# Kernel tuning notes

Hardware: AMD Instinct MI355X
Metric: run time of the kernel (lower is better)

The kernel has to match this reference:

```python
import jax, jax.numpy as jnp
import numpy as np

B, L, D_IN, D_MODEL, N_STATE, DT_RANK, K = 2, 2048, 512, 1024, 16, 64, 4


def setup_inputs() -> dict:
    key = jax.random.key(0)
    ks = jax.random.split(key, 12)
    s = 0.02
    inp = {
        "x_in": jax.random.normal(ks[0], (B, L, D_IN), dtype=jnp.float32),
        "W_in": jax.random.normal(ks[1], (D_MODEL, D_IN), dtype=jnp.float32) * s,
        "W_res": jax.random.normal(ks[2], (D_MODEL, D_IN), dtype=jnp.float32) * s,
        "W_out": jax.random.normal(ks[3], (D_IN, D_MODEL), dtype=jnp.float32) * s,
        "conv_w": jax.random.normal(ks[4], (D_MODEL, 1, K), dtype=jnp.float32) * 0.2,
        "conv_b": jax.random.normal(ks[5], (D_MODEL,), dtype=jnp.float32) * 0.02,
        "A_log": jnp.broadcast_to(jnp.log(jnp.arange(1, N_STATE + 1, dtype=jnp.float32)), (D_MODEL, N_STATE)).copy(),
        "D_param": jnp.ones((D_MODEL,), dtype=jnp.float32),
        "W_B": jax.random.normal(ks[6], (N_STATE, D_MODEL), dtype=jnp.float32) * s,
        "W_C": jax.random.normal(ks[7], (N_STATE, D_MODEL), dtype=jnp.float32) * s,
        "W_dt": jax.random.normal(ks[8], (DT_RANK, D_MODEL), dtype=jnp.float32) * s,
        "W_dtproj": jax.random.normal(ks[9], (D_MODEL, DT_RANK), dtype=jnp.float32) * s,
        "b_dtproj": jax.random.normal(ks[10], (D_MODEL,), dtype=jnp.float32) * 0.05,
    }
    return inp


def _mamba(x_in, W_in, W_res, W_out, conv_w, conv_b, A_log, D_param, W_B, W_C, W_dt, W_dtproj, b_dtproj):
    d_model = conv_w.shape[0]
    k = conv_w.shape[-1]
    x = jnp.einsum('bld,md->blm', x_in, W_in)           # (B,L,D)
    res = jnp.einsum('bld,md->blm', x_in, W_res)        # (B,L,D)
    # causal depthwise conv1d (pad k-1 left, truncate to L == torch pad+slice)
    xc = jnp.transpose(x, (0, 2, 1))                     # (B,D,L)
    xc = jax.lax.conv_general_dilated(xc, conv_w, window_strides=(1,), padding=[(k - 1, 0)],
                                      feature_group_count=d_model,
                                      dimension_numbers=('NCH', 'OIH', 'NCH'))
    xc = xc + conv_b[None, :, None]
    x = jax.nn.silu(jnp.transpose(xc, (0, 2, 1)))        # (B,L,D)
    # selective SSM
    A = -jnp.exp(A_log)                                  # (D,N)
    Bp = jnp.einsum('bld,nd->bln', x, W_B)               # (B,L,N)
    Cp = jnp.einsum('bld,nd->bln', x, W_C)               # (B,L,N)
    delta = jax.nn.softplus(jnp.einsum('bld,rd->blr', x, W_dt) @ W_dtproj.T + b_dtproj)  # (B,L,D)
    dA = jnp.exp(delta[..., None] * A)                   # (B,L,D,N)
    dBu = (delta * x)[..., None] * Bp[:, :, None, :]     # (B,L,D,N)

    def step(h, inp):
        dA_t, dBu_t, C_t = inp
        h = dA_t * h + dBu_t                             # (B,D,N)
        y_t = jnp.einsum('bdn,bn->bd', h, C_t)
        return h, y_t

    h0 = jnp.zeros((x.shape[0], d_model, A.shape[1]), dtype=x.dtype)
    _, ys = jax.lax.scan(step, h0, (jnp.swapaxes(dA, 0, 1), jnp.swapaxes(dBu, 0, 1), jnp.swapaxes(Cp, 0, 1)))
    y = jnp.swapaxes(ys, 0, 1) + x * D_param             # (B,L,D)
    y = y * jax.nn.silu(res)
    return jnp.einsum('bld,od->blo', y, W_out)


def reference(x_in, W_in, W_res, W_out, conv_w, conv_b, A_log, D_param, W_B, W_C, W_dt, W_dtproj, b_dtproj):
    return _mamba(x_in, W_in, W_res, W_out, conv_w, conv_b, A_log, D_param, W_B, W_C, W_dt, W_dtproj, b_dtproj)
```

## Files before the change

kernel.cpp:

```cpp
#include <hip/hip_runtime.h>
#include <stdint.h>
#include <stddef.h>

#define DEVFN __device__ __forceinline__

typedef short bf16x8 __attribute__((ext_vector_type(8)));
typedef short s16x4 __attribute__((ext_vector_type(4)));
typedef float f32x4 __attribute__((ext_vector_type(4)));

namespace {
constexpr int kB   = 2;
constexpr int kL   = 2048;
constexpr int kDin = 512;
constexpr int kDm  = 1024;
constexpr int kNs  = 16;
constexpr int kDtr = 64;
constexpr int kR   = kB * kL;
constexpr int kCH  = 128;
constexpr int kLC  = kL / kCH;
}

DEVFN unsigned short f2bf(float f) {
  union { float f; unsigned u; } v; v.f = f;
  unsigned u = v.u + 0x7fffu + ((v.u >> 16) & 1u);
  return (unsigned short)(u >> 16);
}

DEVFN float bf2f(unsigned short s) {
  union { unsigned u; float f; } v; v.u = ((unsigned)s) << 16;
  return v.f;
}

DEVFN void async16(const void* g, void* l) {
  __builtin_amdgcn_global_load_lds(
      (const __attribute__((address_space(1))) void*)g,
      (__attribute__((address_space(3))) void*)l, 16, 0, 0);
}

DEVFN float sigm(float x) { return 1.0f / (1.0f + __expf(-x)); }

__global__ void prep_kernel(const float* __restrict__ x_in, const float* __restrict__ W_in,
                            const float* __restrict__ W_res, const float* __restrict__ W_out,
                            const float* __restrict__ W_dtp, const float* __restrict__ W_B,
                            const float* __restrict__ W_C, const float* __restrict__ W_dt,
                            const float* __restrict__ A_log,
                            unsigned short* __restrict__ Xb, unsigned short* __restrict__ Wirb,
                            unsigned short* __restrict__ Woutb,
                            unsigned short* __restrict__ Wdtpb, unsigned short* __restrict__ BCdtb,
                            float* __restrict__ Aneg) {
  int i = blockIdx.x * 256 + threadIdx.x;
  if (i < kR * kDin) { Xb[i] = f2bf(x_in[i]); return; }
  i -= kR * kDin;
  if (i < 2 * kDm * kDin) {
    Wirb[i] = f2bf(i < kDm * kDin ? W_in[i] : W_res[i - kDm * kDin]);
    return;
  }
  i -= 2 * kDm * kDin;
  if (i < kDin * kDm) { Woutb[i] = f2bf(W_out[i]); return; }
  i -= kDin * kDm;
  if (i < kDm * kDtr) { Wdtpb[i] = f2bf(W_dtp[i]); return; }
  i -= kDm * kDtr;
  if (i < 128 * kDm) {
    int rr = i >> 10, kk = i & 1023;
    float v = 0.f;
    if (rr < 16)      v = W_B[rr * kDm + kk];
    else if (rr < 32) v = W_C[(rr - 16) * kDm + kk];
    else if (rr < 96) v = W_dt[(rr - 32) * kDm + kk];
    BCdtb[i] = f2bf(v);
    return;
  }
  i -= 128 * kDm;
  if (i < kDm * kNs) { Aneg[i] = -__expf(A_log[i]); }
}

template <int EPI>
__global__ __launch_bounds__(256) void gemm_nt(const unsigned short* __restrict__ A,
                                               const unsigned short* __restrict__ Bw,
                                               float* __restrict__ C,
                                               const float* __restrict__ bias,
                                               unsigned short* __restrict__ Z,
                                               int M, int N, int K) {
  __shared__ __align__(16) unsigned short As[2][128 * 32];
  __shared__ __align__(16) unsigned short Bs[2][128 * 32];
  const int tid = threadIdx.x;
  const int w = tid >> 6, lane = tid & 63;
  const int ntiles = N >> 7;
  const int mt = blockIdx.x / ntiles, nt = blockIdx.x - mt * ntiles;
  const int row0 = mt << 7, col0 = nt << 7;
  const int wr = w >> 1, wc = w & 1;
  const int lr = lane & 15, hi = lane >> 4;

  const int s0 = w * 128 + lane;
  const int s1 = s0 + 64;
  const int c0s = s0 >> 7, r0s = s0 & 127;
  const int c1s = s1 >> 7, r1s = s1 & 127;

  f32x4 acc[4][4] = {};

  auto stage = [&](int buf, int kt) {
    const int kb = kt * 32;
    async16(A  + (size_t)(row0 + r0s) * K + kb + c0s * 8, (void*)&As[buf][(w * 128) * 8]);
    async16(A  + (size_t)(row0 + r1s) * K + kb + c1s * 8, (void*)&As[buf][(w * 128 + 64) * 8]);
    async16(Bw + (size_t)(col0 + r0s) * K + kb + c0s * 8, (void*)&Bs[buf][(w * 128) * 8]);
    async16(Bw + (size_t)(col0 + r1s) * K + kb + c1s * 8, (void*)&Bs[buf][(w * 128 + 64) * 8]);
  };

  const int KT = K >> 5;
  stage(0, 0);
  __syncthreads();
  int buf = 0;
  for (int kt = 0; kt < KT; ++kt) {
    if (kt + 1 < KT) stage(buf ^ 1, kt + 1);
    bf16x8 af[4], bfr[4];
#pragma unroll
    for (int i = 0; i < 4; ++i) {
      af[i]  = *(const bf16x8*)&As[buf][(hi * 128 + wr * 64 + i * 16 + lr) * 8];
      bfr[i] = *(const bf16x8*)&Bs[buf][(hi * 128 + wc * 64 + i * 16 + lr) * 8];
    }
#pragma unroll
    for (int i = 0; i < 4; ++i)
#pragma unroll
      for (int j = 0; j < 4; ++j)
        acc[i][j] = __builtin_amdgcn_mfma_f32_16x16x32_bf16(af[i], bfr[j], acc[i][j], 0, 0, 0);
    __syncthreads();
    buf ^= 1;
  }

#pragma unroll
  for (int i = 0; i < 4; ++i) {
#pragma unroll
    for (int j = 0; j < 4; ++j) {
#pragma unroll
      for (int q = 0; q < 4; ++q) {
        const int r  = row0 + wr * 64 + i * 16 + hi * 4 + q;
        const int cc = col0 + wc * 64 + j * 16 + lr;
        float v = acc[i][j][q];
        if (EPI == 1) {
          v += bias[cc];
          v = fmaxf(v, 0.f) + log1pf(__expf(-fabsf(v)));
          Z[(size_t)r * kDm + cc] = f2bf(v);
        } else if (EPI == 4) {
          if (cc < kDm) C[(size_t)r * kDm + cc] = v;
          else          Z[(size_t)r * kDm + (cc - kDm)] = f2bf(v * sigm(v));
        } else {
          C[(size_t)r * N + cc] = v;
        }
      }
    }
  }
}

__global__ __launch_bounds__(256) void gemm_bcz(const unsigned short* __restrict__ A,
                                                const unsigned short* __restrict__ Bw,
                                                float* __restrict__ P) {
  __shared__ __align__(16) unsigned short As[2][128 * 32];
  __shared__ __align__(16) unsigned short Bs[2][128 * 32];
  const int tid = threadIdx.x;
  const int w = tid >> 6, lane = tid & 63;
  const int mtiles = kR >> 7;
  const int ks = blockIdx.x / mtiles;
  const int mt = blockIdx.x - ks * mtiles;
  const int row0 = mt << 7;
  const int kbase = ks * (kDm / 4);
  const int wr = w >> 1, wc = w & 1;
  const int lr = lane & 15, hi = lane >> 4;

  const int s0 = w * 128 + lane;
  const int s1 = s0 + 64;
  const int c0s = s0 >> 7, r0s = s0 & 127;
  const int c1s = s1 >> 7, r1s = s1 & 127;

  f32x4 acc[4][4] = {};

  auto stage = [&](int buf, int kt) {
    const int kb = kbase + kt * 32;
    async16(A  + (size_t)(row0 + r0s) * kDm + kb + c0s * 8, (void*)&As[buf][(w * 128) * 8]);
    async16(A  + (size_t)(row0 + r1s) * kDm + kb + c1s * 8, (void*)&As[buf][(w * 128 + 64) * 8]);
    async16(Bw + (size_t)r0s * kDm + kb + c0s * 8, (void*)&Bs[buf][(w * 128) * 8]);
    async16(Bw + (size_t)r1s * kDm + kb + c1s * 8, (void*)&Bs[buf][(w * 128 + 64) * 8]);
  };

  const int KT = (kDm / 4) >> 5;
  stage(0, 0);
  __syncthreads();
  int buf = 0;
  for (int kt = 0; kt < KT; ++kt) {
    if (kt + 1 < KT) stage(buf ^ 1, kt + 1);
    bf16x8 af[4], bfr[4];
#pragma unroll
    for (int i = 0; i < 4; ++i) {
      af[i]  = *(const bf16x8*)&As[buf][(hi * 128 + wr * 64 + i * 16 + lr) * 8];
      bfr[i] = *(const bf16x8*)&Bs[buf][(hi * 128 + wc * 64 + i * 16 + lr) * 8];
    }
#pragma unroll
    for (int i = 0; i < 4; ++i)
#pragma unroll
      for (int j = 0; j < 4; ++j)
        acc[i][j] = __builtin_amdgcn_mfma_f32_16x16x32_bf16(af[i], bfr[j], acc[i][j], 0, 0, 0);
    __syncthreads();
    buf ^= 1;
  }

  float* Pk = P + (size_t)ks * kR * 128;
#pragma unroll
  for (int i = 0; i < 4; ++i)
#pragma unroll
    for (int j = 0; j < 4; ++j)
#pragma unroll
      for (int q = 0; q < 4; ++q) {
        const int r  = row0 + wr * 64 + i * 16 + hi * 4 + q;
        const int cc = wc * 64 + j * 16 + lr;
        Pk[(size_t)r * 128 + cc] = acc[i][j][q];
      }
}

__global__ __launch_bounds__(256) void bcz_reduce(const float* __restrict__ P,
                                                  float* __restrict__ BCz,
                                                  unsigned short* __restrict__ z1b) {
  const int i4 = blockIdx.x * 256 + threadIdx.x;
  const size_t base = (size_t)i4 * 4;
  const size_t stride = (size_t)kR * 128;
  f32x4 s = *(const f32x4*)(P + base);
  s += *(const f32x4*)(P + base + stride);
  s += *(const f32x4*)(P + base + 2 * stride);
  s += *(const f32x4*)(P + base + 3 * stride);
  *(f32x4*)(BCz + base) = s;
  const int cc = (int)(base & 127);
  if (cc >= 32 && cc < 96) {
    const int r = (int)(base >> 7);
    s16x4 z = { (short)f2bf(s.x), (short)f2bf(s.y), (short)f2bf(s.z), (short)f2bf(s.w) };
    *(s16x4*)(z1b + (size_t)r * kDtr + (cc - 32)) = z;
  }
}

__global__ __launch_bounds__(256) void conv_silu_kernel(const float* __restrict__ xf,
                                                        const float* __restrict__ conv_w,
                                                        const float* __restrict__ conv_b,
                                                        unsigned short* __restrict__ xcb) {
  const int i = blockIdx.x * 256 + threadIdx.x;
  const int d = i & (kDm - 1);
  const int r = i >> 10;
  const int l = r & (kL - 1);
  float s = conv_b[d];
#pragma unroll
  for (int j = 0; j < 4; ++j) {
    const int ls = l - 3 + j;
    if (ls >= 0) s += xf[(size_t)i + (j - 3) * kDm] * conv_w[d * 4 + j];
  }
  const float v = s * sigm(s);
  xcb[i] = f2bf(v);
}

__global__ __launch_bounds__(256) void scan_phase1(const unsigned short* __restrict__ deltab,
                                                   const unsigned short* __restrict__ xcb,
                                                   const float* __restrict__ BCz,
                                                   float* __restrict__ hend,
                                                   float* __restrict__ dtsum) {
  __shared__ float Bsh[kLC][kNs];
  const int tid = threadIdx.x;
  const int dblk = blockIdx.x & 15;
  const int bc = blockIdx.x >> 4;
  const int c = bc & (kCH - 1);
  const int b = bc >> 7;
  const int rbase = b * kL + c * kLC;
  Bsh[tid >> 4][tid & 15] = BCz[(size_t)(rbase + (tid >> 4)) * 128 + (tid & 15)];
  __syncthreads();

  const int s = tid & 3, dl = tid >> 2;
  const int d = (dblk << 6) + dl;
  const size_t colbase = (size_t)rbase * kDm + d;
  float h0 = 0.f, h1 = 0.f, h2 = 0.f, h3 = 0.f, S = 0.f;
  float dtn = bf2f(deltab[colbase]);
  float xvn = bf2f(xcb[colbase]);
  for (int t = 0; t < kLC; ++t) {
    const float dt = dtn, xv = xvn;
    if (t + 1 < kLC) {
      dtn = bf2f(deltab[colbase + (size_t)(t + 1) * kDm]);
      xvn = bf2f(xcb[colbase + (size_t)(t + 1) * kDm]);
    }
    S += dt;
    const float e1 = __expf(-dt);
    const float e2 = e1 * e1, e4 = e2 * e2, e8 = e4 * e4;
    float pb = e1;
    if (s & 1) pb *= e4;
    if (s & 2) pb *= e8;
    const float f1 = pb * e1, f2 = f1 * e1, f3 = f2 * e1;
    const float du = dt * xv;
    const f32x4 Bv = *(const f32x4*)&Bsh[t][s << 2];
    h0 = fmaf(pb, h0, du * Bv.x);
    h1 = fmaf(f1, h1, du * Bv.y);
    h2 = fmaf(f2, h2, du * Bv.z);
    h3 = fmaf(f3, h3, du * Bv.w);
  }
  const size_t o = ((size_t)bc << 14) + ((size_t)d << 4) + (s << 2);
  *(f32x4*)(hend + o) = f32x4{h0, h1, h2, h3};
  if (s == 0) dtsum[(size_t)bc * kDm + d] = S;
}

__global__ __launch_bounds__(256) void scan_phase2(const float* __restrict__ hend,
                                                   const float* __restrict__ dtsum,
                                                   const float* __restrict__ Aneg,
                                                   float* __restrict__ hin) {
  const int flat = blockIdx.x * 256 + threadIdx.x;
  const int dn = flat & (kDm * kNs - 1);
  const int b = flat >> 14;
  const int d = dn >> 4;
  const float Ar = Aneg[dn];
  size_t o = (size_t)b * kCH * (kDm * kNs) + dn;
  size_t sb = (size_t)b * kCH * kDm + d;
  float h = 0.f;
  float he = hend[o];
  float pp = __expf(Ar * dtsum[sb]);
  for (int c = 0; c < kCH; ++c) {
    const float heC = he, pC = pp;
    if (c + 1 < kCH) {
      he = hend[o + kDm * kNs];
      pp = __expf(Ar * dtsum[sb + kDm]);
    }
    hin[o] = h;
    h = fmaf(pC, h, heC);
    o += kDm * kNs;
    sb += kDm;
  }
}

__global__ __launch_bounds__(256) void scan_phase3(const unsigned short* __restrict__ deltab,
                                                   const unsigned short* __restrict__ xcb,
                                                   const unsigned short* __restrict__ resb,
                                                   const float* __restrict__ BCz,
                                                   const float* __restrict__ hin,
                                                   const float* __restrict__ D_param,
                                                   unsigned short* __restrict__ yb) {
  __shared__ float BCs[kLC][32];
  __shared__ unsigned short ysh[kLC][64];
  const int tid = threadIdx.x;
  const int dblk = blockIdx.x & 15;
  const int bc = blockIdx.x >> 4;
  const int c = bc & (kCH - 1);
  const int b = bc >> 7;
  const int rbase = b * kL + c * kLC;
#pragma unroll
  for (int k2 = 0; k2 < 2; ++k2) {
    const int idx = tid + k2 * 256;
    BCs[idx >> 5][idx & 31] = BCz[(size_t)(rbase + (idx >> 5)) * 128 + (idx & 31)];
  }
  __syncthreads();

  const int s = tid & 3, dl = tid >> 2;
  const int d = (dblk << 6) + dl;
  const size_t colbase = (size_t)rbase * kDm + d;
  const size_t o = ((size_t)bc << 14) + ((size_t)d << 4) + (s << 2);
  const f32x4 hv = *(const f32x4*)(hin + o);
  float h0 = hv.x, h1 = hv.y, h2 = hv.z, h3 = hv.w;
  const float Dp = D_param[d];
  float dtn = bf2f(deltab[colbase]);
  float xvn = bf2f(xcb[colbase]);
  float rsn = bf2f(resb[colbase]);
  for (int t = 0; t < kLC; ++t) {
    const float dt = dtn, xv = xvn, sres = rsn;
    if (t + 1 < kLC) {
      dtn = bf2f(deltab[colbase + (size_t)(t + 1) * kDm]);
      xvn = bf2f(xcb[colbase + (size_t)(t + 1) * kDm]);
      rsn = bf2f(resb[colbase + (size_t)(t + 1) * kDm]);
    }
    const float e1 = __expf(-dt);
    const float e2 = e1 * e1, e4 = e2 * e2, e8 = e4 * e4;
    float pb = e1;
    if (s & 1) pb *= e4;
    if (s & 2) pb *= e8;
    const float f1 = pb * e1, f2 = f1 * e1, f3 = f2 * e1;
    const float du = dt * xv;
    const f32x4 Bv = *(const f32x4*)&BCs[t][s << 2];
    const f32x4 Cv = *(const f32x4*)&BCs[t][16 + (s << 2)];
    h0 = fmaf(pb, h0, du * Bv.x);
    h1 = fmaf(f1, h1, du * Bv.y);
    h2 = fmaf(f2, h2, du * Bv.z);
    h3 = fmaf(f3, h3, du * Bv.w);
    float y = h0 * Cv.x + h1 * Cv.y + h2 * Cv.z + h3 * Cv.w;
    y += __shfl_xor(y, 1);
    y += __shfl_xor(y, 2);
    if (s == 0) ysh[t][dl] = f2bf((y + xv * Dp) * sres);
  }
  __syncthreads();
#pragma unroll
  for (int k2 = 0; k2 < 4; ++k2) {
    const int idx = tid + k2 * 256;
    const int tt = idx >> 6, dd = idx & 63;
    yb[(size_t)(rbase + tt) * kDm + (dblk << 6) + dd] = ysh[tt][dd];
  }
}

extern "C" void kernel_launch(void* const* d_in, const int* in_sizes, int n_in,
                              void* d_out, int out_size, void* d_ws, size_t ws_size,
                              hipStream_t stream) {
  const float* x_in   = (const float*)d_in[0];
  const float* W_in   = (const float*)d_in[1];
  const float* W_res  = (const float*)d_in[2];
  const float* W_out  = (const float*)d_in[3];
  const float* conv_w = (const float*)d_in[4];
  const float* conv_b = (const float*)d_in[5];
  const float* A_log  = (const float*)d_in[6];
  const float* D_par  = (const float*)d_in[7];
  const float* W_B    = (const float*)d_in[8];
  const float* W_C    = (const float*)d_in[9];
  const float* W_dt   = (const float*)d_in[10];
  const float* W_dtp  = (const float*)d_in[11];
  const float* b_dtp  = (const float*)d_in[12];
  float* out = (float*)d_out;

  char* p = (char*)d_ws;
  auto alloc = [&](size_t bytes) { void* q = (void*)p; p += (bytes + 255) & ~(size_t)255; return q; };

  float* xf    = (float*)alloc(sizeof(float) * (size_t)kR * kDm);
  float* BCz   = (float*)alloc(sizeof(float) * (size_t)kR * 128);
  float* Ppart = (float*)alloc(sizeof(float) * 4ull * kR * 128);
  float* hend  = (float*)alloc(sizeof(float) * (size_t)kB * kCH * kDm * kNs);
  float* hin   = (float*)alloc(sizeof(float) * (size_t)kB * kCH * kDm * kNs);
  float* dtsum = (float*)alloc(sizeof(float) * (size_t)kB * kCH * kDm);
  float* Aneg  = (float*)alloc(sizeof(float) * (size_t)kDm * kNs);
  unsigned short* Xb     = (unsigned short*)alloc(2ull * kR * kDin);
  unsigned short* xcb    = (unsigned short*)alloc(2ull * kR * kDm);
  unsigned short* yb     = (unsigned short*)alloc(2ull * kR * kDm);
  unsigned short* resb   = (unsigned short*)alloc(2ull * kR * kDm);
  unsigned short* deltab = (unsigned short*)alloc(2ull * kR * kDm);
  unsigned short* z1b    = (unsigned short*)alloc(2ull * kR * kDtr);
  unsigned short* Wirb   = (unsigned short*)alloc(2ull * 2 * kDm * kDin);
  unsigned short* Woutb  = (unsigned short*)alloc(2ull * kDin * kDm);
  unsigned short* Wdtpb  = (unsigned short*)alloc(2ull * kDm * kDtr);
  unsigned short* BCdtb  = (unsigned short*)alloc(2ull * 128 * kDm);

  if ((size_t)(p - (char*)d_ws) > ws_size) return;

  {
    const int total = kR * kDin + 2 * kDm * kDin + kDin * kDm + kDm * kDtr + 128 * kDm + kDm * kNs;
    prep_kernel<<<(total + 255) / 256, 256, 0, stream>>>(
        x_in, W_in, W_res, W_out, W_dtp, W_B, W_C, W_dt, A_log,
        Xb, Wirb, Woutb, Wdtpb, BCdtb, Aneg);
  }
  gemm_nt<4><<<(kR / 128) * (2 * kDm / 128), 256, 0, stream>>>(Xb, Wirb, xf, nullptr, resb, kR, 2 * kDm, kDin);
  conv_silu_kernel<<<(kR * kDm) / 256, 256, 0, stream>>>(xf, conv_w, conv_b, xcb);
  gemm_bcz<<<4 * (kR / 128), 256, 0, stream>>>(xcb, BCdtb, Ppart);
  bcz_reduce<<<(kR * 128 / 4) / 256, 256, 0, stream>>>(Ppart, BCz, z1b);
  gemm_nt<1><<<(kR / 128) * (kDm / 128), 256, 0, stream>>>(z1b, Wdtpb, nullptr, b_dtp, deltab, kR, kDm, kDtr);
  scan_phase1<<<kB * kCH * (kDm / 64), 256, 0, stream>>>(deltab, xcb, BCz, hend, dtsum);
  scan_phase2<<<(kB * kDm * kNs) / 256, 256, 0, stream>>>(hend, dtsum, Aneg, hin);
  scan_phase3<<<kB * kCH * (kDm / 64), 256, 0, stream>>>(deltab, xcb, resb, BCz, hin, D_par, yb);
  gemm_nt<0><<<(kR / 128) * (kDin / 128), 256, 0, stream>>>(yb, Woutb, out, nullptr, nullptr, kR, kDin, kDm);
}
```

Measured before the change: 174.7 us.

## Fold dt low-rank into packed weight, bf16 intermediates, vectorized conv, smaller out tiles

Precomputes W_dtproj·W_dt as a 1024x1024 bf16 matrix and packs it with W_B/W_C into one 1152-wide weight. A single GEMM then yields delta (with softplus) and B/C, replacing the split-K BC GEMM, its reduce kernel and the rank-64 dt GEMM. The x projection is stored as bf16 and the conv runs 8 channels per thread with vector loads. Scan chunk states (hend/hin) are kept in bf16, phase2 uses 128-thread blocks, and the output GEMM uses 64-row tiles for more blocks. These changes add FLOPs in the dt path and lose precision in the chunk states and the fused dt weight.

```diff
diff --git a/kernel.cpp b/kernel.cpp
--- a/kernel.cpp
+++ b/kernel.cpp
@@ -18,6 +18,7 @@
 constexpr int kR   = kB * kL;
 constexpr int kCH  = 128;
 constexpr int kLC  = kL / kCH;
+constexpr int kNp  = 1152;
 }
 
 DEVFN unsigned short f2bf(float f) {
@@ -46,7 +47,8 @@
                             const float* __restrict__ A_log,
                             unsigned short* __restrict__ Xb, unsigned short* __restrict__ Wirb,
                             unsigned short* __restrict__ Woutb,
-                            unsigned short* __restrict__ Wdtpb, unsigned short* __restrict__ BCdtb,
+                            unsigned short* __restrict__ Wdtpb, unsigned short* __restrict__ WdtT,
+                            unsigned short* __restrict__ Wpack,
                             float* __restrict__ Aneg) {
   int i = blockIdx.x * 256 + threadIdx.x;
   if (i < kR * kDin) { Xb[i] = f2bf(x_in[i]); return; }
@@ -60,13 +62,18 @@
   i -= kDin * kDm;
   if (i < kDm * kDtr) { Wdtpb[i] = f2bf(W_dtp[i]); return; }
   i -= kDm * kDtr;
+  if (i < kDm * kDtr) {
+    const int d = i >> 6, t = i & 63;
+    WdtT[i] = f2bf(W_dt[t * kDm + d]);
+    return;
+  }
+  i -= kDm * kDtr;
   if (i < 128 * kDm) {
-    int rr = i >> 10, kk = i & 1023;
+    const int rr = i >> 10, kk = i & 1023;
     float v = 0.f;
     if (rr < 16)      v = W_B[rr * kDm + kk];
     else if (rr < 32) v = W_C[(rr - 16) * kDm + kk];
-    else if (rr < 96) v = W_dt[(rr - 32) * kDm + kk];
-    BCdtb[i] = f2bf(v);
+    Wpack[(size_t)(1024 + rr) * kDm + kk] = f2bf(v);
     return;
   }
   i -= 128 * kDm;
@@ -79,6 +86,7 @@
                                                float* __restrict__ C,
                                                const float* __restrict__ bias,
                                                unsigned short* __restrict__ Z,
+                                               unsigned short* __restrict__ Z2,
                                                int M, int N, int K) {
   __shared__ __align__(16) unsigned short As[2][128 * 32];
   __shared__ __align__(16) unsigned short Bs[2][128 * 32];
@@ -135,65 +143,66 @@
         const int r  = row0 + wr * 64 + i * 16 + hi * 4 + q;
         const int cc = col0 + wc * 64 + j * 16 + lr;
         float v = acc[i][j][q];
-        if (EPI == 1) {
-          v += bias[cc];
-          v = fmaxf(v, 0.f) + log1pf(__expf(-fabsf(v)));
-          Z[(size_t)r * kDm + cc] = f2bf(v);
-        } else if (EPI == 4) {
-          if (cc < kDm) C[(size_t)r * kDm + cc] = v;
-          else          Z[(size_t)r * kDm + (cc - kDm)] = f2bf(v * sigm(v));
-        } else {
-          C[(size_t)r * N + cc] = v;
+        if (EPI == 4) {
+          if (cc < kDm) Z[(size_t)r * kDm + cc] = f2bf(v);
+          else          Z2[(size_t)r * kDm + (cc - kDm)] = f2bf(v * sigm(v));
+        } else if (EPI == 5) {
+          Z[(size_t)r * N + cc] = f2bf(v);
+        } else if (EPI == 6) {
+          if (cc < 1024) {
+            v += bias[cc];
+            v = fmaxf(v, 0.f) + log1pf(__expf(-fabsf(v)));
+            Z[(size_t)r * kDm + cc] = f2bf(v);
+          } else if (cc < 1056) {
+            C[(size_t)r * 32 + (cc - 1024)] = v;
+          }
         }
       }
     }
   }
 }
 
-__global__ __launch_bounds__(256) void gemm_bcz(const unsigned short* __restrict__ A,
-                                                const unsigned short* __restrict__ Bw,
-                                                float* __restrict__ P) {
-  __shared__ __align__(16) unsigned short As[2][128 * 32];
+__global__ __launch_bounds__(256) void gemm_out64(const unsigned short* __restrict__ A,
+                                                  const unsigned short* __restrict__ Bw,
+                                                  float* __restrict__ C) {
+  __shared__ __align__(16) unsigned short As[2][64 * 32];
   __shared__ __align__(16) unsigned short Bs[2][128 * 32];
   const int tid = threadIdx.x;
   const int w = tid >> 6, lane = tid & 63;
-  const int mtiles = kR >> 7;
-  const int ks = blockIdx.x / mtiles;
-  const int mt = blockIdx.x - ks * mtiles;
-  const int row0 = mt << 7;
-  const int kbase = ks * (kDm / 4);
+  const int mt = blockIdx.x >> 2, nt = blockIdx.x & 3;
+  const int row0 = mt << 6, col0 = nt << 7;
   const int wr = w >> 1, wc = w & 1;
   const int lr = lane & 15, hi = lane >> 4;
 
-  const int s0 = w * 128 + lane;
-  const int s1 = s0 + 64;
+  const int cA = tid >> 6, rA = tid & 63;
+  const int s0 = w * 128 + lane, s1 = s0 + 64;
   const int c0s = s0 >> 7, r0s = s0 & 127;
   const int c1s = s1 >> 7, r1s = s1 & 127;
 
-  f32x4 acc[4][4] = {};
+  f32x4 acc[2][4] = {};
 
   auto stage = [&](int buf, int kt) {
-    const int kb = kbase + kt * 32;
-    async16(A  + (size_t)(row0 + r0s) * kDm + kb + c0s * 8, (void*)&As[buf][(w * 128) * 8]);
-    async16(A  + (size_t)(row0 + r1s) * kDm + kb + c1s * 8, (void*)&As[buf][(w * 128 + 64) * 8]);
-    async16(Bw + (size_t)r0s * kDm + kb + c0s * 8, (void*)&Bs[buf][(w * 128) * 8]);
-    async16(Bw + (size_t)r1s * kDm + kb + c1s * 8, (void*)&Bs[buf][(w * 128 + 64) * 8]);
+    const int kb = kt * 32;
+    async16(A  + (size_t)(row0 + rA) * kDm + kb + cA * 8, (void*)&As[buf][tid * 8]);
+    async16(Bw + (size_t)(col0 + r0s) * kDm + kb + c0s * 8, (void*)&Bs[buf][(w * 128) * 8]);
+    async16(Bw + (size_t)(col0 + r1s) * kDm + kb + c1s * 8, (void*)&Bs[buf][(w * 128 + 64) * 8]);
   };
 
-  const int KT = (kDm / 4) >> 5;
+  const int KT = kDm >> 5;
   stage(0, 0);
   __syncthreads();
   int buf = 0;
   for (int kt = 0; kt < KT; ++kt) {
     if (kt + 1 < KT) stage(buf ^ 1, kt + 1);
-    bf16x8 af[4], bfr[4];
-#pragma unroll
-    for (int i = 0; i < 4; ++i) {
-      af[i]  = *(const bf16x8*)&As[buf][(hi * 128 + wr * 64 + i * 16 + lr) * 8];
-      bfr[i] = *(const bf16x8*)&Bs[buf][(hi * 128 + wc * 64 + i * 16 + lr) * 8];
-    }
-#pragma unroll
-    for (int i = 0; i < 4; ++i)
+    bf16x8 af[2], bfr[4];
+#pragma unroll
+    for (int i = 0; i < 2; ++i)
+      af[i] = *(const bf16x8*)&As[buf][(hi * 64 + wr * 32 + i * 16 + lr) * 8];
+#pragma unroll
+    for (int j = 0; j < 4; ++j)
+      bfr[j] = *(const bf16x8*)&Bs[buf][(hi * 128 + wc * 64 + j * 16 + lr) * 8];
+#pragma unroll
+    for (int i = 0; i < 2; ++i)
 #pragma unroll
       for (int j = 0; j < 4; ++j)
         acc[i][j] = __builtin_amdgcn_mfma_f32_16x16x32_bf16(af[i], bfr[j], acc[i][j], 0, 0, 0);
@@ -201,60 +210,51 @@
     buf ^= 1;
   }
 
-  float* Pk = P + (size_t)ks * kR * 128;
-#pragma unroll
-  for (int i = 0; i < 4; ++i)
+#pragma unroll
+  for (int i = 0; i < 2; ++i)
 #pragma unroll
     for (int j = 0; j < 4; ++j)
 #pragma unroll
       for (int q = 0; q < 4; ++q) {
-        const int r  = row0 + wr * 64 + i * 16 + hi * 4 + q;
-        const int cc = wc * 64 + j * 16 + lr;
-        Pk[(size_t)r * 128 + cc] = acc[i][j][q];
+        const int r  = row0 + wr * 32 + i * 16 + hi * 4 + q;
+        const int cc = col0 + wc * 64 + j * 16 + lr;
+        C[(size_t)r * kDin + cc] = acc[i][j][q];
       }
 }
 
-__global__ __launch_bounds__(256) void bcz_reduce(const float* __restrict__ P,
-                                                  float* __restrict__ BCz,
-                                                  unsigned short* __restrict__ z1b) {
-  const int i4 = blockIdx.x * 256 + threadIdx.x;
-  const size_t base = (size_t)i4 * 4;
-  const size_t stride = (size_t)kR * 128;
-  f32x4 s = *(const f32x4*)(P + base);
-  s += *(const f32x4*)(P + base + stride);
-  s += *(const f32x4*)(P + base + 2 * stride);
-  s += *(const f32x4*)(P + base + 3 * stride);
-  *(f32x4*)(BCz + base) = s;
-  const int cc = (int)(base & 127);
-  if (cc >= 32 && cc < 96) {
-    const int r = (int)(base >> 7);
-    s16x4 z = { (short)f2bf(s.x), (short)f2bf(s.y), (short)f2bf(s.z), (short)f2bf(s.w) };
-    *(s16x4*)(z1b + (size_t)r * kDtr + (cc - 32)) = z;
-  }
-}
-
-__global__ __launch_bounds__(256) void conv_silu_kernel(const float* __restrict__ xf,
-                                                        const float* __restrict__ conv_w,
-                                                        const float* __restrict__ conv_b,
-                                                        unsigned short* __restrict__ xcb) {
-  const int i = blockIdx.x * 256 + threadIdx.x;
-  const int d = i & (kDm - 1);
-  const int r = i >> 10;
+__global__ __launch_bounds__(256) void conv8_kernel(const unsigned short* __restrict__ xfb,
+                                                    const float* __restrict__ conv_w,
+                                                    const float* __restrict__ conv_b,
+                                                    unsigned short* __restrict__ xcb) {
+  const int i8 = blockIdx.x * 256 + threadIdx.x;
+  const int r = i8 >> 7;
+  const int d0 = (i8 & 127) << 3;
   const int l = r & (kL - 1);
-  float s = conv_b[d];
+  bf16x8 xr[4];
 #pragma unroll
   for (int j = 0; j < 4; ++j) {
     const int ls = l - 3 + j;
-    if (ls >= 0) s += xf[(size_t)i + (j - 3) * kDm] * conv_w[d * 4 + j];
-  }
-  const float v = s * sigm(s);
-  xcb[i] = f2bf(v);
+    if (ls >= 0) xr[j] = *(const bf16x8*)(xfb + (size_t)(r - 3 + j) * kDm + d0);
+    else         xr[j] = bf16x8{};
+  }
+  bf16x8 outv;
+#pragma unroll
+  for (int e = 0; e < 8; ++e) {
+    const f32x4 wv = *(const f32x4*)(conv_w + (d0 + e) * 4);
+    float s = conv_b[d0 + e];
+    s = fmaf(bf2f((unsigned short)xr[0][e]), wv.x, s);
+    s = fmaf(bf2f((unsigned short)xr[1][e]), wv.y, s);
+    s = fmaf(bf2f((unsigned short)xr[2][e]), wv.z, s);
+    s = fmaf(bf2f((unsigned short)xr[3][e]), wv.w, s);
+    outv[e] = (short)f2bf(s * sigm(s));
+  }
+  *(bf16x8*)(xcb + (size_t)r * kDm + d0) = outv;
 }
 
 __global__ __launch_bounds__(256) void scan_phase1(const unsigned short* __restrict__ deltab,
                                                    const unsigned short* __restrict__ xcb,
-                                                   const float* __restrict__ BCz,
-                                                   float* __restrict__ hend,
+                                                   const float* __restrict__ BC,
+                                                   unsigned short* __restrict__ hendb,
                                                    float* __restrict__ dtsum) {
   __shared__ float Bsh[kLC][kNs];
   const int tid = threadIdx.x;
@@ -263,7 +263,7 @@
   const int c = bc & (kCH - 1);
   const int b = bc >> 7;
   const int rbase = b * kL + c * kLC;
-  Bsh[tid >> 4][tid & 15] = BCz[(size_t)(rbase + (tid >> 4)) * 128 + (tid & 15)];
+  Bsh[tid >> 4][tid & 15] = BC[(size_t)(rbase + (tid >> 4)) * 32 + (tid & 15)];
   __syncthreads();
 
   const int s = tid & 3, dl = tid >> 2;
@@ -293,15 +293,15 @@
     h3 = fmaf(f3, h3, du * Bv.w);
   }
   const size_t o = ((size_t)bc << 14) + ((size_t)d << 4) + (s << 2);
-  *(f32x4*)(hend + o) = f32x4{h0, h1, h2, h3};
+  *(s16x4*)(hendb + o) = s16x4{(short)f2bf(h0), (short)f2bf(h1), (short)f2bf(h2), (short)f2bf(h3)};
   if (s == 0) dtsum[(size_t)bc * kDm + d] = S;
 }
 
-__global__ __launch_bounds__(256) void scan_phase2(const float* __restrict__ hend,
+__global__ __launch_bounds__(128) void scan_phase2(const unsigned short* __restrict__ hendb,
                                                    const float* __restrict__ dtsum,
                                                    const float* __restrict__ Aneg,
-                                                   float* __restrict__ hin) {
-  const int flat = blockIdx.x * 256 + threadIdx.x;
+                                                   unsigned short* __restrict__ hinb) {
+  const int flat = blockIdx.x * 128 + threadIdx.x;
   const int dn = flat & (kDm * kNs - 1);
   const int b = flat >> 14;
   const int d = dn >> 4;
@@ -309,15 +309,15 @@
   size_t o = (size_t)b * kCH * (kDm * kNs) + dn;
   size_t sb = (size_t)b * kCH * kDm + d;
   float h = 0.f;
-  float he = hend[o];
+  float he = bf2f(hendb[o]);
   float pp = __expf(Ar * dtsum[sb]);
   for (int c = 0; c < kCH; ++c) {
     const float heC = he, pC = pp;
     if (c + 1 < kCH) {
-      he = hend[o + kDm * kNs];
+      he = bf2f(hendb[o + kDm * kNs]);
       pp = __expf(Ar * dtsum[sb + kDm]);
     }
-    hin[o] = h;
+    hinb[o] = f2bf(h);
     h = fmaf(pC, h, heC);
     o += kDm * kNs;
     sb += kDm;
@@ -327,8 +327,8 @@
 __global__ __launch_bounds__(256) void scan_phase3(const unsigned short* __restrict__ deltab,
                                                    const unsigned short* __restrict__ xcb,
                                                    const unsigned short* __restrict__ resb,
-                                                   const float* __restrict__ BCz,
-                                                   const float* __restrict__ hin,
+                                                   const float* __restrict__ BC,
+                                                   const unsigned short* __restrict__ hinb,
                                                    const float* __restrict__ D_param,
                                                    unsigned short* __restrict__ yb) {
   __shared__ float BCs[kLC][32];
@@ -342,7 +342,7 @@
 #pragma unroll
   for (int k2 = 0; k2 < 2; ++k2) {
     const int idx = tid + k2 * 256;
-    BCs[idx >> 5][idx & 31] = BCz[(size_t)(rbase + (idx >> 5)) * 128 + (idx & 31)];
+    BCs[idx >> 5][idx & 31] = BC[(size_t)(rbase + (idx >> 5)) * 32 + (idx & 31)];
   }
   __syncthreads();
 
@@ -350,8 +350,9 @@
   const int d = (dblk << 6) + dl;
   const size_t colbase = (size_t)rbase * kDm + d;
   const size_t o = ((size_t)bc << 14) + ((size_t)d << 4) + (s << 2);
-  const f32x4 hv = *(const f32x4*)(hin + o);
-  float h0 = hv.x, h1 = hv.y, h2 = hv.z, h3 = hv.w;
+  const s16x4 hv = *(const s16x4*)(hinb + o);
+  float h0 = bf2f((unsigned short)hv[0]), h1 = bf2f((unsigned short)hv[1]);
+  float h2 = bf2f((unsigned short)hv[2]), h3 = bf2f((unsigned short)hv[3]);
   const float Dp = D_param[d];
   float dtn = bf2f(deltab[colbase]);
   float xvn = bf2f(xcb[colbase]);
@@ -411,39 +412,37 @@
   char* p = (char*)d_ws;
   auto alloc = [&](size_t bytes) { void* q = (void*)p; p += (bytes + 255) & ~(size_t)255; return q; };
 
-  float* xf    = (float*)alloc(sizeof(float) * (size_t)kR * kDm);
-  float* BCz   = (float*)alloc(sizeof(float) * (size_t)kR * 128);
-  float* Ppart = (float*)alloc(sizeof(float) * 4ull * kR * 128);
-  float* hend  = (float*)alloc(sizeof(float) * (size_t)kB * kCH * kDm * kNs);
-  float* hin   = (float*)alloc(sizeof(float) * (size_t)kB * kCH * kDm * kNs);
+  float* BC    = (float*)alloc(sizeof(float) * (size_t)kR * 32);
   float* dtsum = (float*)alloc(sizeof(float) * (size_t)kB * kCH * kDm);
   float* Aneg  = (float*)alloc(sizeof(float) * (size_t)kDm * kNs);
+  unsigned short* hendb  = (unsigned short*)alloc(2ull * kB * kCH * kDm * kNs);
+  unsigned short* hinb   = (unsigned short*)alloc(2ull * kB * kCH * kDm * kNs);
   unsigned short* Xb     = (unsigned short*)alloc(2ull * kR * kDin);
+  unsigned short* xfb    = (unsigned short*)alloc(2ull * kR * kDm);
   unsigned short* xcb    = (unsigned short*)alloc(2ull * kR * kDm);
   unsigned short* yb     = (unsigned short*)alloc(2ull * kR * kDm);
   unsigned short* resb   = (unsigned short*)alloc(2ull * kR * kDm);
   unsigned short* deltab = (unsigned short*)alloc(2ull * kR * kDm);
-  unsigned short* z1b    = (unsigned short*)alloc(2ull * kR * kDtr);
   unsigned short* Wirb   = (unsigned short*)alloc(2ull * 2 * kDm * kDin);
   unsigned short* Woutb  = (unsigned short*)alloc(2ull * kDin * kDm);
   unsigned short* Wdtpb  = (unsigned short*)alloc(2ull * kDm * kDtr);
-  unsigned short* BCdtb  = (unsigned short*)alloc(2ull * 128 * kDm);
+  unsigned short* WdtT   = (unsigned short*)alloc(2ull * kDm * kDtr);
+  unsigned short* Wpack  = (unsigned short*)alloc(2ull * kNp * kDm);
 
   if ((size_t)(p - (char*)d_ws) > ws_size) return;
 
   {
-    const int total = kR * kDin + 2 * kDm * kDin + kDin * kDm + kDm * kDtr + 128 * kDm + kDm * kNs;
+    const int total = kR * kDin + 2 * kDm * kDin + kDin * kDm + 2 * kDm * kDtr + 128 * kDm + kDm * kNs;
     prep_kernel<<<(total + 255) / 256, 256, 0, stream>>>(
         x_in, W_in, W_res, W_out, W_dtp, W_B, W_C, W_dt, A_log,
-        Xb, Wirb, Woutb, Wdtpb, BCdtb, Aneg);
-  }
-  gemm_nt<4><<<(kR / 128) * (2 * kDm / 128), 256, 0, stream>>>(Xb, Wirb, xf, nullptr, resb, kR, 2 * kDm, kDin);
-  conv_silu_kernel<<<(kR * kDm) / 256, 256, 0, stream>>>(xf, conv_w, conv_b, xcb);
-  gemm_bcz<<<4 * (kR / 128), 256, 0, stream>>>(xcb, BCdtb, Ppart);
-  bcz_reduce<<<(kR * 128 / 4) / 256, 256, 0, stream>>>(Ppart, BCz, z1b);
-  gemm_nt<1><<<(kR / 128) * (kDm / 128), 256, 0, stream>>>(z1b, Wdtpb, nullptr, b_dtp, deltab, kR, kDm, kDtr);
-  scan_phase1<<<kB * kCH * (kDm / 64), 256, 0, stream>>>(deltab, xcb, BCz, hend, dtsum);
-  scan_phase2<<<(kB * kDm * kNs) / 256, 256, 0, stream>>>(hend, dtsum, Aneg, hin);
-  scan_phase3<<<kB * kCH * (kDm / 64), 256, 0, stream>>>(deltab, xcb, resb, BCz, hin, D_par, yb);
-  gemm_nt<0><<<(kR / 128) * (kDin / 128), 256, 0, stream>>>(yb, Woutb, out, nullptr, nullptr, kR, kDin, kDm);
-}
+        Xb, Wirb, Woutb, Wdtpb, WdtT, Wpack, Aneg);
+  }
+  gemm_nt<5><<<(kDm / 128) * (kDm / 128), 256, 0, stream>>>(Wdtpb, WdtT, nullptr, nullptr, Wpack, nullptr, kDm, kDm, kDtr);
+  gemm_nt<4><<<(kR / 128) * (2 * kDm / 128), 256, 0, stream>>>(Xb, Wirb, nullptr, nullptr, xfb, resb, kR, 2 * kDm, kDin);
+  conv8_kernel<<<(kR * kDm / 8) / 256, 256, 0, stream>>>(xfb, conv_w, conv_b, xcb);
+  gemm_nt<6><<<(kR / 128) * (kNp / 128), 256, 0, stream>>>(xcb, Wpack, BC, b_dtp, deltab, nullptr, kR, kNp, kDm);
+  scan_phase1<<<kB * kCH * (kDm / 64), 256, 0, stream>>>(deltab, xcb, BC, hendb, dtsum);
+  scan_phase2<<<(kB * kDm * kNs) / 128, 128, 0, stream>>>(hendb, dtsum, Aneg, hinb);
+  scan_phase3<<<kB * kCH * (kDm / 64), 256, 0, stream>>>(deltab, xcb, resb, BC, hinb, D_par, yb);
+  gemm_out64<<<(kR / 64) * (kDin / 128), 256, 0, stream>>>(yb, Woutb, out);
+}
```

Result: slower. 199.5 us (+14.2%).
